# Kernel tuning notes

Hardware: AMD Instinct MI355X
Metric: run time of the kernel (lower is better)

The kernel has to match this reference:

```python
import jax, jax.numpy as jnp
import numpy as np


def setup_inputs() -> dict:
    key = jax.random.key(0)
    ks = jax.random.split(key, 6)
    B, Lq, Lm, D = 4, 2048, 2048, 1024
    s = D ** -0.5
    return {
        "input": jax.random.normal(ks[0], (B, Lq, D), jnp.float32),
        "memory": jax.random.normal(ks[1], (B, Lm, D), jnp.float32),
        # torch Linear weights are [out_features, in_features]
        "Wq": jax.random.normal(ks[2], (D, D), jnp.float32) * s,
        "Wk": jax.random.normal(ks[3], (D, D), jnp.float32) * s,
        "Wv": jax.random.normal(ks[4], (D, D), jnp.float32) * s,
        "Wo": jax.random.normal(ks[5], (D, D), jnp.float32) * s,
    }


def reference(input, memory, Wq, Wk, Wv, Wo):
    # q/k/v projections (Linear, no bias): x @ W.T
    depth = Wq.shape[0]
    q = jnp.einsum("bqd,ed->bqe", input, Wq) * (depth ** -0.5)
    k = jnp.einsum("bmd,ed->bme", memory, Wk)
    v = jnp.einsum("bmd,ed->bme", memory, Wv)
    logit = jnp.einsum("bqe,bme->bqm", q, k)          # [B, Lq, Lm]
    attention_weight = jax.nn.softmax(logit, axis=-1)
    attention_output = jnp.einsum("bqm,bme->bqe", attention_weight, v)
    return jnp.einsum("bqe,oe->bqo", attention_output, Wo)
```

## Files before the change

kernel.cpp:

```cpp
#include <hip/hip_runtime.h>
#include <hip/hip_bf16.h>

typedef unsigned short u16;
typedef __bf16 bf16x8 __attribute__((ext_vector_type(8)));
typedef float floatx4 __attribute__((ext_vector_type(4)));
typedef __hip_bfloat16 bf;

__device__ __forceinline__ __bf16 f2b(float f) {
    __hip_bfloat16 h = __float2bfloat16(f);
    return *reinterpret_cast<__bf16*>(&h);
}
__device__ __forceinline__ bf16x8 ld8f(const float* p) {
    float4 a = ((const float4*)p)[0];
    float4 b = ((const float4*)p)[1];
    bf16x8 r;
    r[0] = f2b(a.x); r[1] = f2b(a.y); r[2] = f2b(a.z); r[3] = f2b(a.w);
    r[4] = f2b(b.x); r[5] = f2b(b.y); r[6] = f2b(b.z); r[7] = f2b(b.w);
    return r;
}
__device__ __forceinline__ void storev(float* p, float v) { *p = v; }
__device__ __forceinline__ void storev(bf* p, float v)    { *p = __float2bfloat16(v); }

__device__ __forceinline__ void gl16(const bf* g, u16* l) {
    __builtin_amdgcn_global_load_lds(
        (const __attribute__((address_space(1))) void*)g,
        (__attribute__((address_space(3))) void*)l, 16, 0, 0);
}

__device__ __forceinline__ void swz3(int& bx, int& by, int& bz) {
    const int nx = gridDim.x, ny = gridDim.y, nz = gridDim.z;
    const int lid = blockIdx.x + nx * (blockIdx.y + ny * blockIdx.z);
    const int cpx = (nx * ny * nz) >> 3;
    const int s = (lid & 7) * cpx + (lid >> 3);
    bx = s % nx;
    const int r = s / nx;
    by = r % ny;
    bz = r / ny;
}

#define FENCE asm volatile("" ::: "memory")
#define BARx  __builtin_amdgcn_s_barrier()
#define VM3   asm volatile("s_waitcnt vmcnt(3)" ::: "memory")
#define VM6   asm volatile("s_waitcnt vmcnt(6)" ::: "memory")
#define VM0   asm volatile("s_waitcnt vmcnt(0)" ::: "memory")
#define SP1   __builtin_amdgcn_s_setprio(1)
#define SP0   __builtin_amdgcn_s_setprio(0)



#define ST_A2(u, kt, Ab) \
    gl16(Asrc + (long)((u) * 64) * K + (long)(kt) * 64, (Ab) + (u) * 4096 + tid * 8)
#define ST_B2(u, kt, Bb) \
    gl16(Bsrc + (long)((u) * 64) * K + (long)(kt) * 64, (Bb) + (u) * 4096 + tid * 8)

#define RD_A2(dst, h, Ab) do { _Pragma("unroll") \
    for (int q_ = 0; q_ < 4; q_++) { \
        const u16* p_ = (Ab) + (wg * 128 + (h) * 64 + q_ * 16 + fr) * 64; \
        dst[q_ * 2 + 0] = *(const bf16x8*)(p_ + kl0); \
        dst[q_ * 2 + 1] = *(const bf16x8*)(p_ + kl1); \
    } } while (0)

#define RD_B2(dst, c, Bb) do { _Pragma("unroll") \
    for (int j_ = 0; j_ < 2; j_++) { \
        const u16* p_ = (Bb) + (w4 * 64 + (c) * 32 + j_ * 16 + fr) * 64; \
        dst[j_ * 2 + 0] = *(const bf16x8*)(p_ + kl0); \
        dst[j_ * 2 + 1] = *(const bf16x8*)(p_ + kl1); \
    } } while (0)

#define QMM2(h, c, av, bv) do { _Pragma("unroll") \
    for (int q_ = 0; q_ < 4; q_++) _Pragma("unroll") \
    for (int j_ = 0; j_ < 2; j_++) _Pragma("unroll") \
    for (int kk_ = 0; kk_ < 2; kk_++) \
        acc[(h) * 4 + q_][(c) * 2 + j_] = __builtin_amdgcn_mfma_f32_16x16x32_bf16( \
            av[q_ * 2 + kk_], bv[j_ * 2 + kk_], acc[(h) * 4 + q_][(c) * 2 + j_], 0, 0, 0); \
} while (0)

template <typename OutT>
__device__ __forceinline__ void gemm256_core(
    const bf* __restrict__ A, const bf* __restrict__ B, OutT* __restrict__ C,
    int K, int N, int m_blk, int n_blk, float scale, u16* lds)
{
    const int tid = threadIdx.x;
    const int w = tid >> 6, lane = tid & 63;
    const int wg = w >> 2, w4 = w & 3;
    const int fr = lane & 15, kg = lane >> 4;

    u16* const A0b = lds;
    u16* const B0b = lds + 16384;
    u16* const A1b = lds + 32768;
    u16* const B1b = lds + 49152;

    const int kl0 = (kg * 8) ^ ((fr & 7) << 3);
    const int kl1 = kl0 ^ 32;

    const int sr  = tid >> 3;
    const int scs = ((tid & 7) * 8) ^ ((sr & 7) << 3);
    const bf* Asrc = A + (long)(m_blk + sr) * K + scs;
    const bf* Bsrc = B + (long)(n_blk + sr) * K + scs;

    floatx4 acc[8][4];
#pragma unroll
    for (int i = 0; i < 8; i++)
#pragma unroll
        for (int j = 0; j < 4; j++) acc[i][j] = (floatx4){0.f, 0.f, 0.f, 0.f};

    bf16x8 a[8], b0[4], b1[4];

    const int T     = K >> 6;
    const int iters = T >> 1;

#pragma unroll
    for (int u = 0; u < 4; u++) { ST_A2(u, 0, A0b); ST_B2(u, 0, B0b); }
#pragma unroll
    for (int u = 0; u < 4; u++) { ST_A2(u, 1, A1b); ST_B2(u, 1, B1b); }
    VM0; BARx; FENCE;

    for (int it = 0; it < iters; ++it) {
        const int t   = it * 2;
        const int ts0 = (t + 2 < T) ? t + 2 : 0;
        const int ts1 = (t + 3 < T) ? t + 3 : 0;

        RD_A2(a, 0, A0b); RD_B2(b0, 0, B0b);
        if (it) { ST_A2(1, t + 1, A1b); ST_A2(3, t + 1, A1b); }
        SP1; QMM2(0, 0, a, b0); SP0;
        FENCE; BARx; FENCE;

        RD_B2(b1, 1, B0b);
        ST_A2(0, ts0, A0b); ST_A2(2, ts0, A0b);
        SP1; QMM2(0, 1, a, b1); SP0;
        FENCE; BARx; FENCE;

        RD_A2(a, 1, A0b);
        ST_B2(0, ts0, B0b); ST_B2(1, ts0, B0b);
        SP1; QMM2(1, 1, a, b1); SP0;
        FENCE; BARx; FENCE;

        ST_B2(2, ts0, B0b); ST_B2(3, ts0, B0b);
        SP1; QMM2(1, 0, a, b0); SP0;
        VM6; BARx; FENCE;

        RD_A2(a, 0, A1b); RD_B2(b0, 0, B1b);
        ST_A2(1, ts0, A0b); ST_A2(3, ts0, A0b);
        SP1; QMM2(0, 0, a, b0); SP0;
        FENCE; BARx; FENCE;

        RD_B2(b1, 1, B1b);
        ST_A2(0, ts1, A1b); ST_A2(2, ts1, A1b);
        SP1; QMM2(0, 1, a, b1); SP0;
        FENCE; BARx; FENCE;

        RD_A2(a, 1, A1b);
        ST_B2(0, ts1, B1b); ST_B2(1, ts1, B1b);
        SP1; QMM2(1, 1, a, b1); SP0;
        FENCE; BARx; FENCE;

        ST_B2(2, ts1, B1b); ST_B2(3, ts1, B1b);
        SP1; QMM2(1, 0, a, b0); SP0;
        VM6; BARx; FENCE;
    }

    const long c_col0 = n_blk + w4 * 64 + fr;
    const long c_row0 = m_blk + wg * 128 + (lane >> 4) * 4;
#pragma unroll
    for (int rf = 0; rf < 8; rf++)
#pragma unroll
        for (int r = 0; r < 4; r++) {
            const long row = c_row0 + rf * 16 + r;
#pragma unroll
            for (int cf = 0; cf < 4; cf++)
                storev(&C[row * N + c_col0 + cf * 16], acc[rf][cf][r] * scale);
        }
}

template <typename OutT>
__global__ __launch_bounds__(512)
void gemm256(const bf* __restrict__ A, const bf* __restrict__ B,
             OutT* __restrict__ C, int K, int N,
             long sA, long sB, long sC, float scale)
{
    __shared__ __align__(16) u16 lds[65536];
    int bx, by, bz; swz3(bx, by, bz);
    gemm256_core(A + bz * sA, B + bz * sB, C + bz * sC,
                 K, N, by * 256, bx * 256, scale, lds);
}

__global__ __launch_bounds__(512)
void gemm256_qk(const bf* __restrict__ xb, const bf* __restrict__ memb,
                const bf* __restrict__ Wqb, const bf* __restrict__ Wkb,
                bf* __restrict__ Q, bf* __restrict__ Kp, float qscale)
{
    __shared__ __align__(16) u16 lds[65536];
    int bx, by, bz; swz3(bx, by, bz);
    gemm256_core(bz ? memb : xb, bz ? Wkb : Wqb, bz ? Kp : Q, 1024, 1024,
                 by * 256, bx * 256, bz ? 1.f : qscale, lds);
}


#define ST_A(h, kt, Ab) \
    gl16(Asrc + (long)((h) * 32) * K + (long)(kt) * 64, (Ab) + (h) * 4096 + tid * 8)
#define ST_Bu0(c, kt, Bb) \
    gl16(Bsrc + (long)((c) * 32) * K + (long)(kt) * 64, (Bb) + (c) * 8192 + tid * 8)
#define ST_Bu1(c, kt, Bb) \
    gl16(Bsrc + (long)((c) * 32 + 128) * K + (long)(kt) * 64, (Bb) + (c) * 8192 + 4096 + tid * 8)

#define RD_A(dst, h, Ab) do { _Pragma("unroll") \
    for (int q_ = 0; q_ < 2; q_++) { \
        const u16* p_ = (Ab) + ((h) * 64 + wg * 32 + q_ * 16 + fr) * 64; \
        dst[q_ * 2 + 0] = *(const bf16x8*)(p_ + kl0); \
        dst[q_ * 2 + 1] = *(const bf16x8*)(p_ + kl1); \
    } } while (0)

#define RD_B(dst, c, Bb) do { _Pragma("unroll") \
    for (int j_ = 0; j_ < 2; j_++) { \
        const u16* p_ = (Bb) + ((c) * 128 + w4 * 32 + j_ * 16 + fr) * 64; \
        dst[j_ * 2 + 0] = *(const bf16x8*)(p_ + kl0); \
        dst[j_ * 2 + 1] = *(const bf16x8*)(p_ + kl1); \
    } } while (0)

#define QMM(h, c, av, bv) do { _Pragma("unroll") \
    for (int q_ = 0; q_ < 2; q_++) _Pragma("unroll") \
    for (int j_ = 0; j_ < 2; j_++) _Pragma("unroll") \
    for (int kk_ = 0; kk_ < 2; kk_++) \
        acc[(h) * 2 + q_][(c) * 2 + j_] = __builtin_amdgcn_mfma_f32_16x16x32_bf16( \
            av[q_ * 2 + kk_], bv[j_ * 2 + kk_], acc[(h) * 2 + q_][(c) * 2 + j_], 0, 0, 0); \
} while (0)

template <typename OutT>
__device__ __forceinline__ void gemm128_core(
    const bf* __restrict__ A, const bf* __restrict__ B, OutT* __restrict__ C,
    int K, int N, int m_blk, int n_blk, float scale, u16* lds)
{
    const int tid  = threadIdx.x;
    const int w    = tid >> 6, lane = tid & 63;
    const int wg   = w >> 2, w4 = w & 3;
    const int fr   = lane & 15, kg = lane >> 4;

    u16* const A0b = lds;
    u16* const B0b = lds + 8192;
    u16* const A1b = lds + 24576;
    u16* const B1b = lds + 32768;

    const int kl0 = (kg * 8) ^ ((fr & 7) << 3);
    const int kl1 = kl0 ^ 32;

    const int sr  = tid >> 3;
    const int scs = ((tid & 7) * 8) ^ ((sr & 7) << 3);
    const bf* Asrc = A + (long)(m_blk + (tid >> 8) * 64 + (sr & 31)) * K + scs;
    const bf* Bsrc = B + (long)(n_blk + (tid >> 8) * 64 + (sr & 31)) * K + scs;

    floatx4 acc[4][4];
#pragma unroll
    for (int i = 0; i < 4; i++)
#pragma unroll
        for (int j = 0; j < 4; j++) acc[i][j] = (floatx4){0.f, 0.f, 0.f, 0.f};

    bf16x8 a0[4], a1[4], b0[4], b1[4];

    const int T     = K >> 6;
    const int iters = T >> 1;

    ST_A(0, 0, A0b); ST_A(1, 0, A0b);
    ST_Bu0(0, 0, B0b); ST_Bu1(0, 0, B0b); ST_Bu0(1, 0, B0b); ST_Bu1(1, 0, B0b);
    ST_A(0, 1, A1b); ST_A(1, 1, A1b);
    ST_Bu0(0, 1, B1b); ST_Bu1(0, 1, B1b); ST_Bu0(1, 1, B1b); ST_Bu1(1, 1, B1b);
    VM0; BARx; FENCE;

    for (int it = 0; it < iters; ++it) {
        const int t   = it * 2;
        const int ts0 = (t + 2 < T) ? t + 2 : 0;
        const int ts1 = (t + 3 < T) ? t + 3 : 0;

        RD_A(a0, 0, A0b); RD_A(a1, 1, A0b); RD_B(b0, 0, B0b);
        if (it) { ST_Bu1(0, t + 1, B1b); ST_Bu0(1, t + 1, B1b); ST_Bu1(1, t + 1, B1b); }
        SP1; QMM(0, 0, a0, b0); QMM(1, 0, a1, b0); SP0;
        FENCE; BARx; FENCE;

        RD_B(b1, 1, B0b);
        ST_A(0, ts0, A0b); ST_A(1, ts0, A0b); ST_Bu0(0, ts0, B0b);
        SP1; QMM(0, 1, a0, b1); QMM(1, 1, a1, b1); SP0;
        VM3; BARx; FENCE;

        RD_A(a0, 0, A1b); RD_A(a1, 1, A1b); RD_B(b0, 0, B1b);
        ST_Bu1(0, ts0, B0b); ST_Bu0(1, ts0, B0b); ST_Bu1(1, ts0, B0b);
        SP1; QMM(0, 0, a0, b0); QMM(1, 0, a1, b0); SP0;
        FENCE; BARx; FENCE;

        RD_B(b1, 1, B1b);
        ST_A(0, ts1, A1b); ST_A(1, ts1, A1b); ST_Bu0(0, ts1, B1b);
        SP1; QMM(0, 1, a0, b1); QMM(1, 1, a1, b1); SP0;
        VM3; BARx; FENCE;
    }

    const long c_col0 = n_blk + w4 * 64 + fr;
    const long c_row0 = m_blk + wg * 64 + (lane >> 4) * 4;
#pragma unroll
    for (int rf = 0; rf < 4; rf++)
#pragma unroll
        for (int r = 0; r < 4; r++) {
            const long row = c_row0 + rf * 16 + r;
#pragma unroll
            for (int cf = 0; cf < 4; cf++)
                storev(&C[row * N + c_col0 + cf * 16], acc[rf][cf][r] * scale);
        }
}

template <typename OutT>
__global__ __launch_bounds__(512)
void gemm128(const bf* __restrict__ A, const bf* __restrict__ B,
             OutT* __restrict__ C, int K, int N,
             long sA, long sB, long sC, float scale)
{
    __shared__ __align__(16) u16 lds[49152];
    int bx, by, bz; swz3(bx, by, bz);
    gemm128_core(A + bz * sA, B + bz * sB, C + bz * sC,
                 K, N, by * 128, bx * 256, scale, lds);
}

__global__ __launch_bounds__(256)
void cvt2(const float* __restrict__ a, const float* __restrict__ b,
          bf* __restrict__ da, bf* __restrict__ db, long n)
{
    const float* s = blockIdx.z ? b : a;
    bf* d = blockIdx.z ? db : da;
    const long stride = (long)gridDim.x * 256;
    for (long i = (long)blockIdx.x * 256 + threadIdx.x; i * 8 < n; i += stride)
        *(bf16x8*)(d + i * 8) = ld8f(s + i * 8);
}

__global__ __launch_bounds__(256)
void cvt_w(const float* __restrict__ w0, const float* __restrict__ w1,
           const float* __restrict__ w2, const float* __restrict__ w3,
           bf* __restrict__ d)
{
    const int z = blockIdx.z;
    const float* s = (z == 0) ? w0 : (z == 1) ? w1 : (z == 2) ? w2 : w3;
    bf* dz = d + (long)z * (1 << 20);
    const long i = ((long)blockIdx.x * 256 + threadIdx.x) * 8;
    *(bf16x8*)(dz + i) = ld8f(s + i);
}

__global__ __launch_bounds__(256)
void softmax_rows_2048(bf* __restrict__ X)
{
    const long row = blockIdx.x;
    const int t = threadIdx.x;
    const int wave = t >> 6, lane = t & 63;
    __shared__ float red[8];

    float v[8];
    float m = -1e30f;
#pragma unroll
    for (int i = 0; i < 8; i++) {
        v[i] = __bfloat162float(X[row * 2048 + t + i * 256]);
        m = fmaxf(m, v[i]);
    }
#pragma unroll
    for (int o = 32; o > 0; o >>= 1) m = fmaxf(m, __shfl_xor(m, o, 64));
    if (lane == 0) red[wave] = m;
    __syncthreads();
    m = fmaxf(fmaxf(red[0], red[1]), fmaxf(red[2], red[3]));

    float s = 0.f;
#pragma unroll
    for (int i = 0; i < 8; i++) { v[i] = __expf(v[i] - m); s += v[i]; }
#pragma unroll
    for (int o = 32; o > 0; o >>= 1) s += __shfl_xor(s, o, 64);
    if (lane == 0) red[4 + wave] = s;
    __syncthreads();
    s = red[4] + red[5] + red[6] + red[7];

    const float inv = 1.f / s;
#pragma unroll
    for (int i = 0; i < 8; i++)
        X[row * 2048 + t + i * 256] = __float2bfloat16(v[i] * inv);
}

extern "C" void kernel_launch(void* const* d_in, const int* in_sizes, int n_in,
                              void* d_out, int out_size, void* d_ws, size_t ws_size,
                              hipStream_t stream)
{
    const float* x   = (const float*)d_in[0];
    const float* mem = (const float*)d_in[1];
    const float* Wq  = (const float*)d_in[2];
    const float* Wk  = (const float*)d_in[3];
    const float* Wv  = (const float*)d_in[4];
    const float* Wo  = (const float*)d_in[5];

    constexpr int  B = 4, L = 2048, D = 1024;
    constexpr long LD = (long)L * D;
    constexpr long LL = (long)L * L;
    constexpr size_t CH = 1u << 24;

    char* ws = (char*)d_ws;
    bf* Q   = (bf*)(ws + 0 * CH);
    bf* Kp  = (bf*)(ws + 1 * CH);
    bf* Vt  = (bf*)(ws + 2 * CH);
    bf* Wb  = (bf*)(ws + 3 * CH);
    bf* Wqb = Wb;
    bf* Wkb = Wb + (long)(1 << 20);
    bf* Wvb = Wb + (long)2 * (1 << 20);
    bf* Wob = Wb + (long)3 * (1 << 20);
    bf* AO  = Q;

    bf* xb   = (bf*)d_out;
    bf* memb = (bf*)d_out + B * LD;
    bf* Lg   = (bf*)d_out;

    const float qscale = 0.03125f;

    cvt2<<<dim3(1024, 1, 2), dim3(256), 0, stream>>>(x, mem, xb, memb, B * LD);
    cvt_w<<<dim3(512, 1, 4), dim3(256), 0, stream>>>(Wq, Wk, Wv, Wo, Wb);

    gemm256_qk<<<dim3(4, 32, 2), dim3(512), 0, stream>>>(
        xb, memb, Wqb, Wkb, Q, Kp, qscale);

    gemm128<bf><<<dim3(8, 8, 4), dim3(512), 0, stream>>>(
        Wvb, memb, Vt, D, L, 0, LD, (long)D * L, 1.f);

    gemm256<bf><<<dim3(8, 8, 4), dim3(512), 0, stream>>>(
        Q, Kp, Lg, D, L, LD, LD, LL, 1.f);

    softmax_rows_2048<<<dim3(B * L), dim3(256), 0, stream>>>(Lg);

    gemm128<bf><<<dim3(4, 16, 4), dim3(512), 0, stream>>>(
        Lg, Vt, AO, L, D, LL, (long)D * L, LD, 1.f);

    gemm128<float><<<dim3(4, 64, 1), dim3(512), 0, stream>>>(
        AO, Wob, (float*)d_out, D, D, 0, 0, 0, 1.f);
}
```

Baseline: 285.3 us.

## Stage GEMM tile loads through registers instead of direct global-to-LDS loads

Replaces the global_load_lds direct copies in the 256-tile bf16 GEMM with uint4 global loads into registers, which are written to LDS one MFMA phase later, and changes the barrier waits to lgkmcnt(0). It also drops the separate b0/b1 fragment buffers, so B fragments are re-read from LDS instead of kept in registers. The goal is finer control over load/write scheduling and lower register pressure. In exchange, each global load now has only about one MFMA phase to hide its latency before the compiler must wait on it for the ds_write. It also adds extra LDS write and read traffic.

```diff
diff --git a/kernel.cpp b/kernel.cpp
--- a/kernel.cpp
+++ b/kernel.cpp
@@ -40,18 +40,12 @@
 
 #define FENCE asm volatile("" ::: "memory")
 #define BARx  __builtin_amdgcn_s_barrier()
+#define LGKM0 asm volatile("s_waitcnt lgkmcnt(0)" ::: "memory")
 #define VM3   asm volatile("s_waitcnt vmcnt(3)" ::: "memory")
-#define VM6   asm volatile("s_waitcnt vmcnt(6)" ::: "memory")
 #define VM0   asm volatile("s_waitcnt vmcnt(0)" ::: "memory")
 #define SP1   __builtin_amdgcn_s_setprio(1)
 #define SP0   __builtin_amdgcn_s_setprio(0)
 
-
-
-#define ST_A2(u, kt, Ab) \
-    gl16(Asrc + (long)((u) * 64) * K + (long)(kt) * 64, (Ab) + (u) * 4096 + tid * 8)
-#define ST_B2(u, kt, Bb) \
-    gl16(Bsrc + (long)((u) * 64) * K + (long)(kt) * 64, (Bb) + (u) * 4096 + tid * 8)
 
 #define RD_A2(dst, h, Ab) do { _Pragma("unroll") \
     for (int q_ = 0; q_ < 4; q_++) { \
@@ -75,6 +69,10 @@
             av[q_ * 2 + kk_], bv[j_ * 2 + kk_], acc[(h) * 4 + q_][(c) * 2 + j_], 0, 0, 0); \
 } while (0)
 
+#define LD_AU(r, u, kt) (r) = *(const uint4*)(Asrc + (long)((u) * 64) * K + (long)(kt) * 64)
+#define LD_BU(r, u, kt) (r) = *(const uint4*)(Bsrc + (long)((u) * 64) * K + (long)(kt) * 64)
+#define WRU(buf, u, r)  *(uint4*)((buf) + (u) * 4096 + tid * 8) = (r)
+
 template <typename OutT>
 __device__ __forceinline__ void gemm256_core(
     const bf* __restrict__ A, const bf* __restrict__ B, OutT* __restrict__ C,
@@ -104,59 +102,68 @@
 #pragma unroll
         for (int j = 0; j < 4; j++) acc[i][j] = (floatx4){0.f, 0.f, 0.f, 0.f};
 
-    bf16x8 a[8], b0[4], b1[4];
+    bf16x8 a[8], b[4];
+    uint4 pA, pB, qA, qB;
 
     const int T     = K >> 6;
     const int iters = T >> 1;
 
 #pragma unroll
-    for (int u = 0; u < 4; u++) { ST_A2(u, 0, A0b); ST_B2(u, 0, B0b); }
-#pragma unroll
-    for (int u = 0; u < 4; u++) { ST_A2(u, 1, A1b); ST_B2(u, 1, B1b); }
-    VM0; BARx; FENCE;
+    for (int u = 0; u < 4; u++) {
+        uint4 ra, rb; LD_AU(ra, u, 0); LD_BU(rb, u, 0);
+        WRU(A0b, u, ra); WRU(B0b, u, rb);
+    }
+#pragma unroll
+    for (int u = 0; u < 4; u++) {
+        uint4 ra, rb; LD_AU(ra, u, 1); LD_BU(rb, u, 1);
+        WRU(A1b, u, ra); WRU(B1b, u, rb);
+    }
+    LGKM0; BARx; FENCE;
 
     for (int it = 0; it < iters; ++it) {
         const int t   = it * 2;
         const int ts0 = (t + 2 < T) ? t + 2 : 0;
         const int ts1 = (t + 3 < T) ? t + 3 : 0;
 
-        RD_A2(a, 0, A0b); RD_B2(b0, 0, B0b);
-        if (it) { ST_A2(1, t + 1, A1b); ST_A2(3, t + 1, A1b); }
-        SP1; QMM2(0, 0, a, b0); SP0;
-        FENCE; BARx; FENCE;
-
-        RD_B2(b1, 1, B0b);
-        ST_A2(0, ts0, A0b); ST_A2(2, ts0, A0b);
-        SP1; QMM2(0, 1, a, b1); SP0;
-        FENCE; BARx; FENCE;
+        RD_A2(a, 0, A0b); RD_B2(b, 0, B0b);
+        if (it) { WRU(B1b, 0, pA); WRU(B1b, 1, pB); }
+        LD_AU(pA, 0, ts0); LD_AU(pB, 2, ts0);
+        SP1; QMM2(0, 0, a, b); SP0; LGKM0; BARx; FENCE;
+
+        RD_B2(b, 1, B0b);
+        if (it) { WRU(B1b, 2, qA); WRU(B1b, 3, qB); }
+        LD_AU(qA, 1, ts0); LD_AU(qB, 3, ts0);
+        SP1; QMM2(0, 1, a, b); SP0; LGKM0; BARx; FENCE;
 
         RD_A2(a, 1, A0b);
-        ST_B2(0, ts0, B0b); ST_B2(1, ts0, B0b);
-        SP1; QMM2(1, 1, a, b1); SP0;
-        FENCE; BARx; FENCE;
-
-        ST_B2(2, ts0, B0b); ST_B2(3, ts0, B0b);
-        SP1; QMM2(1, 0, a, b0); SP0;
-        VM6; BARx; FENCE;
-
-        RD_A2(a, 0, A1b); RD_B2(b0, 0, B1b);
-        ST_A2(1, ts0, A0b); ST_A2(3, ts0, A0b);
-        SP1; QMM2(0, 0, a, b0); SP0;
-        FENCE; BARx; FENCE;
-
-        RD_B2(b1, 1, B1b);
-        ST_A2(0, ts1, A1b); ST_A2(2, ts1, A1b);
-        SP1; QMM2(0, 1, a, b1); SP0;
-        FENCE; BARx; FENCE;
+        WRU(A0b, 0, pA); WRU(A0b, 2, pB);
+        LD_BU(pA, 0, ts0); LD_BU(pB, 1, ts0);
+        SP1; QMM2(1, 1, a, b); SP0; LGKM0; BARx; FENCE;
+
+        RD_B2(b, 0, B0b);
+        WRU(A0b, 1, qA); WRU(A0b, 3, qB);
+        LD_BU(qA, 2, ts0); LD_BU(qB, 3, ts0);
+        SP1; QMM2(1, 0, a, b); SP0; LGKM0; BARx; FENCE;
+
+        RD_A2(a, 0, A1b); RD_B2(b, 0, B1b);
+        WRU(B0b, 0, pA); WRU(B0b, 1, pB);
+        LD_AU(pA, 0, ts1); LD_AU(pB, 2, ts1);
+        SP1; QMM2(0, 0, a, b); SP0; LGKM0; BARx; FENCE;
+
+        RD_B2(b, 1, B1b);
+        WRU(B0b, 2, qA); WRU(B0b, 3, qB);
+        LD_AU(qA, 1, ts1); LD_AU(qB, 3, ts1);
+        SP1; QMM2(0, 1, a, b); SP0; LGKM0; BARx; FENCE;
 
         RD_A2(a, 1, A1b);
-        ST_B2(0, ts1, B1b); ST_B2(1, ts1, B1b);
-        SP1; QMM2(1, 1, a, b1); SP0;
-        FENCE; BARx; FENCE;
-
-        ST_B2(2, ts1, B1b); ST_B2(3, ts1, B1b);
-        SP1; QMM2(1, 0, a, b0); SP0;
-        VM6; BARx; FENCE;
+        WRU(A1b, 0, pA); WRU(A1b, 2, pB);
+        LD_BU(pA, 0, ts1); LD_BU(pB, 1, ts1);
+        SP1; QMM2(1, 1, a, b); SP0; LGKM0; BARx; FENCE;
+
+        RD_B2(b, 0, B1b);
+        WRU(A1b, 1, qA); WRU(A1b, 3, qB);
+        LD_BU(qA, 2, ts1); LD_BU(qB, 3, ts1);
+        SP1; QMM2(1, 0, a, b); SP0; LGKM0; BARx; FENCE;
     }
 
     const long c_col0 = n_blk + w4 * 64 + fr;
```

Measured after the change: 296.4 us. +3.9%, slower.
